# Optimization experiments

Measured on AMD Instinct MI355X. Metric: run time of the kernel, lower is better.

The kernel has to match this reference:

```python
import jax, jax.numpy as jnp
import numpy as np
import math

D_MODEL = 1024
N_HEAD = 16


def _layer_norm(x, w, b, eps=1e-5):
    mu = jnp.mean(x, axis=-1, keepdims=True)
    var = jnp.var(x, axis=-1, keepdims=True)
    return (x - mu) * jax.lax.rsqrt(var + eps) * w + b


def setup_inputs() -> dict:
    key = jax.random.key(0)
    ks = jax.random.split(key, 8)
    d = D_MODEL
    s = 0.02
    return {
        "x": jax.random.normal(ks[0], (2, 2048, d), dtype=jnp.float32),
        "ln1_w": jnp.ones((d,), jnp.float32),
        "ln1_b": jnp.zeros((d,), jnp.float32),
        "qkv_w": jax.random.normal(ks[1], (d, 3 * d), jnp.float32) * s,
        "qkv_b": jnp.zeros((3 * d,), jnp.float32),
        "attn_out_w": jax.random.normal(ks[2], (d, d), jnp.float32) * s,
        "attn_out_b": jnp.zeros((d,), jnp.float32),
        "ln2_w": jnp.ones((d,), jnp.float32),
        "ln2_b": jnp.zeros((d,), jnp.float32),
        "c_fc_w": jax.random.normal(ks[3], (d, 4 * d), jnp.float32) * s,
        "c_fc_b": jnp.zeros((4 * d,), jnp.float32),
        "c_proj_w": jax.random.normal(ks[4], (4 * d, d), jnp.float32) * s,
        "c_proj_b": jnp.zeros((d,), jnp.float32),
    }


def _block(x, ln1_w, ln1_b, qkv_w, qkv_b, attn_out_w, attn_out_b,
           ln2_w, ln2_b, c_fc_w, c_fc_b, c_proj_w, c_proj_b):
    B, S, D = x.shape
    H = N_HEAD
    hd = D // H

    # pre-LN (NOTE: original code overwrites x with ln_1(x), so the
    # attention residual is around the *normalized* input)
    xn = _layer_norm(x, ln1_w, ln1_b)

    qkv = xn @ qkv_w + qkv_b                       # [B,S,3D]
    q, k, v = jnp.split(qkv, 3, axis=-1)
    q = q.reshape(B, S, H, hd).transpose(0, 2, 1, 3)  # [B,H,S,hd]
    k = k.reshape(B, S, H, hd).transpose(0, 2, 1, 3)
    v = v.reshape(B, S, H, hd).transpose(0, 2, 1, 3)

    scale = 1.0 / math.sqrt(hd)
    scores = jnp.einsum("bhqd,bhkd->bhqk", q, k) * scale
    causal = jnp.tril(jnp.ones((S, S), dtype=bool))
    scores = jnp.where(causal, scores, -jnp.inf)
    attn = jax.nn.softmax(scores, axis=-1)
    o = jnp.einsum("bhqk,bhkd->bhqd", attn, v)
    o = o.transpose(0, 2, 1, 3).reshape(B, S, D)
    o = o @ attn_out_w + attn_out_b                # attention output

    h = xn + o                                     # residual around ln_1 output
    hn = _layer_norm(h, ln2_w, ln2_b)
    mlp = jax.nn.gelu(hn @ c_fc_w + c_fc_b, approximate=False) @ c_proj_w + c_proj_b
    return hn + mlp                                # residual around ln_2 output


def reference(x, ln1_w, ln1_b, qkv_w, qkv_b, attn_out_w, attn_out_b,
              ln2_w, ln2_b, c_fc_w, c_fc_b, c_proj_w, c_proj_b):
    return _block(x, ln1_w, ln1_b, qkv_w, qkv_b, attn_out_w, attn_out_b,
                  ln2_w, ln2_b, c_fc_w, c_fc_b, c_proj_w, c_proj_b)
```

## Files before the change

kernel.cpp:

```cpp
#include <hip/hip_runtime.h>
#include <math.h>

#define D_MODEL 1024
#define SEQ     2048
#define BATCH   2
#define NHEAD   16
#define ROWS    (BATCH*SEQ)

typedef __attribute__((ext_vector_type(8))) short  bf16x8;
typedef __attribute__((ext_vector_type(4))) float  f32x4;

__device__ __forceinline__ float bf2f(short u) {
    union { unsigned int i; float f; } x;
    x.i = ((unsigned int)(unsigned short)u) << 16;
    return x.f;
}
__device__ __forceinline__ short f2bf(float f) {
    unsigned int u = __float_as_uint(f);
    unsigned int r = (u + 0x7FFFu + ((u >> 16) & 1u)) >> 16;
    return (short)r;
}
__device__ __forceinline__ unsigned int packbf2(float a, float b) {
    return (unsigned int)(unsigned short)f2bf(a)
         | ((unsigned int)(unsigned short)f2bf(b) << 16);
}
__device__ __forceinline__ void gload_lds16(const void* g, void* l) {
    __builtin_amdgcn_global_load_lds(
        (const __attribute__((address_space(1))) unsigned int*)g,
        (__attribute__((address_space(3))) unsigned int*)l, 16, 0, 0);
}
__device__ __forceinline__ float wave_sum(float v) {
#pragma unroll
    for (int o = 32; o > 0; o >>= 1) v += __shfl_xor(v, o, 64);
    return v;
}

__global__ __launch_bounds__(256) void ln_kernel(
    const float* __restrict__ in, const float* __restrict__ w,
    const float* __restrict__ b, float* __restrict__ outF,
    short* __restrict__ outB)
{
    const int row = blockIdx.x;
    const int tid = threadIdx.x;
    const float4 v = ((const float4*)(in + (size_t)row * D_MODEL))[tid];
    float s  = v.x + v.y + v.z + v.w;
    float ss = v.x*v.x + v.y*v.y + v.z*v.z + v.w*v.w;
    s  = wave_sum(s);
    ss = wave_sum(ss);
    __shared__ float red[2][4];
    const int wid = tid >> 6, lane = tid & 63;
    if (lane == 0) { red[0][wid] = s; red[1][wid] = ss; }
    __syncthreads();
    const float ts  = red[0][0] + red[0][1] + red[0][2] + red[0][3];
    const float tss = red[1][0] + red[1][1] + red[1][2] + red[1][3];
    const float mean = ts * (1.0f / D_MODEL);
    const float var  = tss * (1.0f / D_MODEL) - mean * mean;
    const float inv  = rsqrtf(var + 1e-5f);
    const float4 wv = ((const float4*)w)[tid];
    const float4 bv = ((const float4*)b)[tid];
    float o0 = (v.x - mean) * inv * wv.x + bv.x;
    float o1 = (v.y - mean) * inv * wv.y + bv.y;
    float o2 = (v.z - mean) * inv * wv.z + bv.z;
    float o3 = (v.w - mean) * inv * wv.w + bv.w;
    if (outF) {
        float4 o = make_float4(o0, o1, o2, o3);
        ((float4*)(outF + (size_t)row * D_MODEL))[tid] = o;
    }
    ushort4 ob;
    ob.x = (unsigned short)f2bf(o0); ob.y = (unsigned short)f2bf(o1);
    ob.z = (unsigned short)f2bf(o2); ob.w = (unsigned short)f2bf(o3);
    ((ushort4*)(outB + (size_t)row * D_MODEL))[tid] = ob;
}

__global__ __launch_bounds__(256) void wprep(
    const float* __restrict__ W, short* __restrict__ Wt, int K, int N)
{
    __shared__ float t[32][33];
    const int kk = blockIdx.y << 5, nn = blockIdx.x << 5;
    const int r = threadIdx.x >> 3, c = (threadIdx.x & 7) << 2;
    const float4 v = *(const float4*)(W + (size_t)(kk + r) * N + nn + c);
    t[r][c + 0] = v.x; t[r][c + 1] = v.y; t[r][c + 2] = v.z; t[r][c + 3] = v.w;
    __syncthreads();
    ushort4 o;
    o.x = (unsigned short)f2bf(t[c + 0][r]);
    o.y = (unsigned short)f2bf(t[c + 1][r]);
    o.z = (unsigned short)f2bf(t[c + 2][r]);
    o.w = (unsigned short)f2bf(t[c + 3][r]);
    *(ushort4*)(Wt + (size_t)(nn + r) * K + kk + c) = o;
}

__global__ __launch_bounds__(256) void reduce2(
    const float* __restrict__ p0, const float* __restrict__ p1,
    const float* __restrict__ bias, const float* __restrict__ res,
    float* __restrict__ o, int N)
{
    const size_t i = (size_t)blockIdx.x * 256 + threadIdx.x;
    const float4 a = ((const float4*)p0)[i];
    const float4 b = ((const float4*)p1)[i];
    const int col = (int)((i << 2) & (size_t)(N - 1));
    const float4 bb = *(const float4*)(bias + col);
    const float4 r = ((const float4*)res)[i];
    float4 v;
    v.x = a.x + b.x + bb.x + r.x;
    v.y = a.y + b.y + bb.y + r.y;
    v.z = a.z + b.z + bb.z + r.z;
    v.w = a.w + b.w + bb.w + r.w;
    ((float4*)o)[i] = v;
}

template<bool GELU>
__global__ __launch_bounds__(256) void gemm_mfma(
    const short* __restrict__ A, const short* __restrict__ Bt,
    const float* __restrict__ bias, const float* __restrict__ res,
    float* __restrict__ outF, float* __restrict__ outF2,
    short* __restrict__ outB, int M, int N, int Klen, int lda)
{
    __shared__ short As[2][128 * 32];
    __shared__ short Bs[2][128 * 32];
    const int tid = threadIdx.x;
    const int wid = tid >> 6, lane = tid & 63;
    const int wm = wid >> 1, wn = wid & 1;
    const int m0 = blockIdx.y << 7, n0 = blockIdx.x << 7;
    const int kbeg = blockIdx.z * Klen;

    const int srow = lane >> 2;
    const int sseg = (lane & 3) << 3;
    const short* Ag = A  + (size_t)(m0 + (wid << 5) + srow) * lda + kbeg + sseg;
    const short* Bg = Bt + (size_t)(n0 + (wid << 5) + srow) * lda + kbeg + sseg;
    const int wb = wid << 10;

#define STAGE(buf, k0) do { \
        gload_lds16(Ag + (k0),                    &As[buf][wb]);        \
        gload_lds16(Ag + (size_t)16 * lda + (k0), &As[buf][wb + 512]);  \
        gload_lds16(Bg + (k0),                    &Bs[buf][wb]);        \
        gload_lds16(Bg + (size_t)16 * lda + (k0), &Bs[buf][wb + 512]);  \
    } while (0)

    f32x4 acc[4][4];
#pragma unroll
    for (int i = 0; i < 4; ++i)
#pragma unroll
        for (int j = 0; j < 4; ++j) acc[i][j] = (f32x4){0.f, 0.f, 0.f, 0.f};

    const int frow = lane & 15;
    const int kb   = (lane >> 4) << 3;

    STAGE(0, 0);
    int cur = 0;
    for (int k0 = 0; k0 < Klen; k0 += 32) {
        __syncthreads();
        if (k0 + 32 < Klen) STAGE(cur ^ 1, k0 + 32);

        bf16x8 af[4], bfr[4];
#pragma unroll
        for (int mt = 0; mt < 4; ++mt)
            af[mt] = *(const bf16x8*)
                &As[cur][((wm << 6) + (mt << 4) + frow) << 5 | kb];
#pragma unroll
        for (int nt = 0; nt < 4; ++nt)
            bfr[nt] = *(const bf16x8*)
                &Bs[cur][((wn << 6) + (nt << 4) + frow) << 5 | kb];
#pragma unroll
        for (int mt = 0; mt < 4; ++mt)
#pragma unroll
            for (int nt = 0; nt < 4; ++nt)
                acc[mt][nt] = __builtin_amdgcn_mfma_f32_16x16x32_bf16(
                    af[mt], bfr[nt], acc[mt][nt], 0, 0, 0);
        cur ^= 1;
    }
#undef STAGE

    const int lrow = (lane >> 4) << 2;
    const int lcol = lane & 15;
    if (outF2) {
        float* po = (blockIdx.z == 0) ? outF : outF2;
#pragma unroll
        for (int nt = 0; nt < 4; ++nt) {
            const int col = n0 + (wn << 6) + (nt << 4) + lcol;
#pragma unroll
            for (int mt = 0; mt < 4; ++mt)
#pragma unroll
                for (int r = 0; r < 4; ++r) {
                    const int row = m0 + (wm << 6) + (mt << 4) + lrow + r;
                    po[(size_t)row * N + col] = acc[mt][nt][r];
                }
        }
        return;
    }
#pragma unroll
    for (int nt = 0; nt < 4; ++nt) {
        const int col = n0 + (wn << 6) + (nt << 4) + lcol;
        const float bb = bias[col];
#pragma unroll
        for (int mt = 0; mt < 4; ++mt) {
#pragma unroll
            for (int r = 0; r < 4; ++r) {
                const int row = m0 + (wm << 6) + (mt << 4) + lrow + r;
                float v = acc[mt][nt][r] + bb;
                if (GELU) v = 0.5f * v * (1.0f + erff(v * 0.70710678118654752f));
                if (res)  v += res[(size_t)row * N + col];
                if (outF) outF[(size_t)row * N + col] = v;
                if (outB) outB[(size_t)row * N + col] = f2bf(v);
            }
        }
    }
}

__global__ __launch_bounds__(256) void attn3(
    const short* __restrict__ qkv,
    short* __restrict__ o)
{
    const int qb = blockIdx.x & 31;
    const int bh = blockIdx.x >> 5;
    const int b = bh >> 4, h = bh & 15;
    const int tid = threadIdx.x;
    const int w = tid >> 6, lane = tid & 63;
    const int g = lane >> 4, fr = lane & 15;
    const int qbase = qb << 6;

    __shared__ short Ks[64 * 64];
    __shared__ short Vt[64 * 72];
    __shared__ short Ps[4 * 16 * 72];

    const size_t qrow = (size_t)(b * SEQ + qbase + (w << 4) + fr);
    const short* qp = qkv + qrow * 3072 + h * 64 + (g << 3);
    const bf16x8 qf0 = *(const bf16x8*)qp;
    const bf16x8 qf1 = *(const bf16x8*)(qp + 32);

    f32x4 oT[4];
#pragma unroll
    for (int i = 0; i < 4; ++i) oT[i] = (f32x4){0.f, 0.f, 0.f, 0.f};
    float lsum = 0.f;

    const int krow = lane >> 3, kseg = lane & 7;
    const int kpair = tid & 31, vd0 = (tid >> 5) << 3;
    short* PsW = &Ps[(w << 4) * 72];
    const int qloc = (w << 4) + fr;

    for (int t = 0; t <= qb; ++t) {
        const int k0 = t << 6;
        __syncthreads();
        {
            const int key0 = (w << 4) + krow;
            const int sw = (kseg ^ krow) << 3;
            const short* kgp = qkv + (size_t)(b * SEQ + k0 + key0) * 3072
                               + 1024 + h * 64 + sw;
            gload_lds16(kgp,                 &Ks[((w << 4) + 0) << 6]);
            gload_lds16(kgp + (size_t)8 * 3072, &Ks[((w << 4) + 8) << 6]);
        }
        {
            const short* vp = qkv + (size_t)(b * SEQ + k0 + (kpair << 1)) * 3072
                              + 2048 + h * 64 + vd0;
            const bf16x8 va = *(const bf16x8*)vp;
            const bf16x8 vb = *(const bf16x8*)(vp + 3072);
#pragma unroll
            for (int i = 0; i < 8; ++i)
                *(unsigned int*)&Vt[(vd0 + i) * 72 + (kpair << 1)] =
                    (unsigned int)(unsigned short)va[i]
                    | ((unsigned int)(unsigned short)vb[i] << 16);
        }
        __syncthreads();

        f32x4 sT[4];
#pragma unroll
        for (int i = 0; i < 4; ++i) sT[i] = (f32x4){0.f, 0.f, 0.f, 0.f};
#pragma unroll
        for (int kh = 0; kh < 2; ++kh) {
            const bf16x8 qf = kh ? qf1 : qf0;
            const int tseg = g + (kh << 2);
#pragma unroll
            for (int mt = 0; mt < 4; ++mt) {
                const int key = (mt << 4) + fr;
                const bf16x8 kf = *(const bf16x8*)
                    &Ks[(key << 6) + ((tseg ^ (key & 7)) << 3)];
                sT[mt] = __builtin_amdgcn_mfma_f32_16x16x32_bf16(
                    kf, qf, sT[mt], 0, 0, 0);
            }
        }

        const bool diag = (t == qb);
#pragma unroll
        for (int mt = 0; mt < 4; ++mt) {
            float p0 = __expf(0.125f * sT[mt][0]);
            float p1 = __expf(0.125f * sT[mt][1]);
            float p2 = __expf(0.125f * sT[mt][2]);
            float p3 = __expf(0.125f * sT[mt][3]);
            if (diag) {
                const int key = (mt << 4) + (g << 2);
                if (key + 0 > qloc) p0 = 0.f;
                if (key + 1 > qloc) p1 = 0.f;
                if (key + 2 > qloc) p2 = 0.f;
                if (key + 3 > qloc) p3 = 0.f;
            }
            lsum += (p0 + p1) + (p2 + p3);
            *(uint2*)&PsW[fr * 72 + (mt << 4) + (g << 2)] =
                make_uint2(packbf2(p0, p1), packbf2(p2, p3));
        }

#pragma unroll
        for (int kh = 0; kh < 2; ++kh) {
            const bf16x8 pf = *(const bf16x8*)
                &PsW[fr * 72 + (g << 3) + (kh << 5)];
#pragma unroll
            for (int mt = 0; mt < 4; ++mt) {
                const bf16x8 vf = *(const bf16x8*)
                    &Vt[((mt << 4) + fr) * 72 + (g << 3) + (kh << 5)];
                oT[mt] = __builtin_amdgcn_mfma_f32_16x16x32_bf16(
                    vf, pf, oT[mt], 0, 0, 0);
            }
        }
    }

    lsum += __shfl_xor(lsum, 16, 64);
    lsum += __shfl_xor(lsum, 32, 64);
    const float rl = 1.0f / lsum;
    short* orow = o + qrow * D_MODEL + h * 64;
#pragma unroll
    for (int mt = 0; mt < 4; ++mt) {
        *(uint2*)&orow[(mt << 4) + (g << 2)] = make_uint2(
            packbf2(oT[mt][0] * rl, oT[mt][1] * rl),
            packbf2(oT[mt][2] * rl, oT[mt][3] * rl));
    }
}

extern "C" void kernel_launch(void* const* d_in, const int* in_sizes, int n_in,
                              void* d_out, int out_size, void* d_ws, size_t ws_size,
                              hipStream_t stream) {
    const float* x          = (const float*)d_in[0];
    const float* ln1_w      = (const float*)d_in[1];
    const float* ln1_b      = (const float*)d_in[2];
    const float* qkv_w      = (const float*)d_in[3];
    const float* qkv_b      = (const float*)d_in[4];
    const float* attn_out_w = (const float*)d_in[5];
    const float* attn_out_b = (const float*)d_in[6];
    const float* ln2_w      = (const float*)d_in[7];
    const float* ln2_b      = (const float*)d_in[8];
    const float* c_fc_w     = (const float*)d_in[9];
    const float* c_fc_b     = (const float*)d_in[10];
    const float* c_proj_w   = (const float*)d_in[11];
    const float* c_proj_b   = (const float*)d_in[12];
    float* out = (float*)d_out;

    char* W = (char*)d_ws;
    float* xn_f   = (float*)W;
    char*  poolA  = W + 16777216;
    short* xn_b   = (short*)poolA;
    short* qkvbuf = (short*)(poolA + 8388608);
    short* attn_b = (short*)poolA;
    short* fc_b   = (short*)poolA;
    short* hn_b   = (short*)(poolA + 33554432);
    short* wts    = (short*)(poolA + 33554432 + 8388608);
    short* qkvw_t = wts;
    short* attnw_t= wts + 3145728;
    short* fcw_t  = wts + 4194304;
    short* projw_t= wts + 8388608;
    float* cp_p0  = xn_f;
    float* cp_p1  = (float*)(W + 50331648);

    const dim3 blk(256);

    wprep<<<dim3(3072/32, 1024/32), blk, 0, stream>>>(qkv_w, qkvw_t, 1024, 3072);
    wprep<<<dim3(1024/32, 1024/32), blk, 0, stream>>>(attn_out_w, attnw_t, 1024, 1024);
    wprep<<<dim3(4096/32, 1024/32), blk, 0, stream>>>(c_fc_w, fcw_t, 1024, 4096);
    wprep<<<dim3(1024/32, 4096/32), blk, 0, stream>>>(c_proj_w, projw_t, 4096, 1024);

    ln_kernel<<<ROWS, blk, 0, stream>>>(x, ln1_w, ln1_b, xn_f, xn_b);
    gemm_mfma<false><<<dim3(24, 32), blk, 0, stream>>>(
        xn_b, qkvw_t, qkv_b, nullptr, nullptr, nullptr, qkvbuf,
        ROWS, 3072, 1024, 1024);
    attn3<<<dim3(32 * 32), blk, 0, stream>>>(qkvbuf, attn_b);
    gemm_mfma<false><<<dim3(8, 32), blk, 0, stream>>>(
        attn_b, attnw_t, attn_out_b, xn_f, xn_f, nullptr, nullptr,
        ROWS, 1024, 1024, 1024);
    ln_kernel<<<ROWS, blk, 0, stream>>>(xn_f, ln2_w, ln2_b, out, hn_b);
    gemm_mfma<true><<<dim3(32, 32), blk, 0, stream>>>(
        hn_b, fcw_t, c_fc_b, nullptr, nullptr, nullptr, fc_b,
        ROWS, 4096, 1024, 1024);
    gemm_mfma<false><<<dim3(8, 32, 2), blk, 0, stream>>>(
        fc_b, projw_t, nullptr, nullptr, cp_p0, cp_p1, nullptr,
        ROWS, 1024, 2048, 4096);
    reduce2<<<dim3(ROWS * 1024 / 4 / 256), blk, 0, stream>>>(
        cp_p0, cp_p1, c_proj_b, out, out, 1024);
}
```

Baseline: 423.2 us.

## Pipeline GEMM with vmcnt waits, XCD-aware block remap, LDS-staged bf16 epilogue

```diff
diff --git a/kernel.cpp b/kernel.cpp
--- a/kernel.cpp
+++ b/kernel.cpp
@@ -115,12 +115,16 @@
     float* __restrict__ outF, float* __restrict__ outF2,
     short* __restrict__ outB, int M, int N, int Klen, int lda)
 {
-    __shared__ short As[2][128 * 32];
-    __shared__ short Bs[2][128 * 32];
+    __shared__ short smem[16384];
     const int tid = threadIdx.x;
     const int wid = tid >> 6, lane = tid & 63;
     const int wm = wid >> 1, wn = wid & 1;
-    const int m0 = blockIdx.y << 7, n0 = blockIdx.x << 7;
+
+    const int gx = gridDim.x;
+    const int nwg = gx * gridDim.y;
+    int wg = blockIdx.y * gx + blockIdx.x;
+    wg = (wg & 7) * (nwg >> 3) + (wg >> 3);
+    const int m0 = (wg / gx) << 7, n0 = (wg % gx) << 7;
     const int kbeg = blockIdx.z * Klen;
 
     const int srow = lane >> 2;
@@ -130,10 +134,12 @@
     const int wb = wid << 10;
 
 #define STAGE(buf, k0) do { \
-        gload_lds16(Ag + (k0),                    &As[buf][wb]);        \
-        gload_lds16(Ag + (size_t)16 * lda + (k0), &As[buf][wb + 512]);  \
-        gload_lds16(Bg + (k0),                    &Bs[buf][wb]);        \
-        gload_lds16(Bg + (size_t)16 * lda + (k0), &Bs[buf][wb + 512]);  \
+        short* As_ = smem + ((buf) << 12) + wb;        \
+        short* Bs_ = smem + 8192 + ((buf) << 12) + wb; \
+        gload_lds16(Ag + (k0),                    As_);        \
+        gload_lds16(Ag + (size_t)16 * lda + (k0), As_ + 512);  \
+        gload_lds16(Bg + (k0),                    Bs_);        \
+        gload_lds16(Bg + (size_t)16 * lda + (k0), Bs_ + 512);  \
     } while (0)
 
     f32x4 acc[4][4];
@@ -146,32 +152,38 @@
     const int kb   = (lane >> 4) << 3;
 
     STAGE(0, 0);
+    STAGE(1, 32);
     int cur = 0;
     for (int k0 = 0; k0 < Klen; k0 += 32) {
-        __syncthreads();
-        if (k0 + 32 < Klen) STAGE(cur ^ 1, k0 + 32);
+        if (k0 + 32 < Klen) asm volatile("s_waitcnt vmcnt(4)" ::: "memory");
+        else                asm volatile("s_waitcnt vmcnt(0)" ::: "memory");
+        asm volatile("s_barrier" ::: "memory");
 
         bf16x8 af[4], bfr[4];
+        const int ab = (cur << 12) + kb;
+        const int bb = 8192 + (cur << 12) + kb;
 #pragma unroll
         for (int mt = 0; mt < 4; ++mt)
-            af[mt] = *(const bf16x8*)
-                &As[cur][((wm << 6) + (mt << 4) + frow) << 5 | kb];
+            af[mt] = *(const bf16x8*)&smem[ab + (((wm << 6) + (mt << 4) + frow) << 5)];
 #pragma unroll
         for (int nt = 0; nt < 4; ++nt)
-            bfr[nt] = *(const bf16x8*)
-                &Bs[cur][((wn << 6) + (nt << 4) + frow) << 5 | kb];
+            bfr[nt] = *(const bf16x8*)&smem[bb + (((wn << 6) + (nt << 4) + frow) << 5)];
 #pragma unroll
         for (int mt = 0; mt < 4; ++mt)
 #pragma unroll
             for (int nt = 0; nt < 4; ++nt)
                 acc[mt][nt] = __builtin_amdgcn_mfma_f32_16x16x32_bf16(
                     af[mt], bfr[nt], acc[mt][nt], 0, 0, 0);
+
+        asm volatile("s_barrier" ::: "memory");
+        if (k0 + 64 < Klen) STAGE(cur, k0 + 64);
         cur ^= 1;
     }
 #undef STAGE
 
     const int lrow = (lane >> 4) << 2;
     const int lcol = lane & 15;
+
     if (outF2) {
         float* po = (blockIdx.z == 0) ? outF : outF2;
 #pragma unroll
@@ -187,20 +199,47 @@
         }
         return;
     }
+
+    if (outB) {
+        __syncthreads();
+#pragma unroll
+        for (int nt = 0; nt < 4; ++nt) {
+            const int cl = (wn << 6) + (nt << 4) + lcol;
+            const float bv = bias[n0 + cl];
+#pragma unroll
+            for (int mt = 0; mt < 4; ++mt)
+#pragma unroll
+                for (int r = 0; r < 4; ++r) {
+                    const int rl = (wm << 6) + (mt << 4) + lrow + r;
+                    float v = acc[mt][nt][r] + bv;
+                    if (GELU) v = 0.5f * v * (1.0f + erff(v * 0.70710678118654752f));
+                    smem[(rl << 7) + (cl ^ (((rl >> 2) & 3) << 4))] = f2bf(v);
+                }
+        }
+        __syncthreads();
+        const int row = tid >> 1, c0 = (tid & 1) << 6;
+        const int sw = ((row >> 2) & 3) << 4;
+        short* gp = outB + (size_t)(m0 + row) * N + n0 + c0;
+#pragma unroll
+        for (int j = 0; j < 8; ++j)
+            *(uint4*)(gp + (j << 3)) =
+                *(const uint4*)&smem[(row << 7) + ((c0 + (j << 3)) ^ sw)];
+        return;
+    }
+
 #pragma unroll
     for (int nt = 0; nt < 4; ++nt) {
         const int col = n0 + (wn << 6) + (nt << 4) + lcol;
-        const float bb = bias[col];
+        const float bv = bias[col];
 #pragma unroll
         for (int mt = 0; mt < 4; ++mt) {
 #pragma unroll
             for (int r = 0; r < 4; ++r) {
                 const int row = m0 + (wm << 6) + (mt << 4) + lrow + r;
-                float v = acc[mt][nt][r] + bb;
+                float v = acc[mt][nt][r] + bv;
                 if (GELU) v = 0.5f * v * (1.0f + erff(v * 0.70710678118654752f));
                 if (res)  v += res[(size_t)row * N + col];
-                if (outF) outF[(size_t)row * N + col] = v;
-                if (outB) outB[(size_t)row * N + col] = f2bf(v);
+                outF[(size_t)row * N + col] = v;
             }
         }
     }
@@ -210,8 +249,10 @@
     const short* __restrict__ qkv,
     short* __restrict__ o)
 {
-    const int qb = blockIdx.x & 31;
-    const int bh = blockIdx.x >> 5;
+    int wg = blockIdx.x;
+    wg = (wg & 7) * 128 + (wg >> 3);
+    const int qb = wg & 31;
+    const int bh = wg >> 5;
     const int b = bh >> 4, h = bh & 15;
     const int tid = threadIdx.x;
     const int w = tid >> 6, lane = tid & 63;
```

Result: faster. 407.7 us (-3.7%).
